# Performance work log

Measured on AMD Instinct MI355X. Metric: run time of the kernel, lower is better.

The kernel has to match this reference:

```python
import jax, jax.numpy as jnp
import numpy as np

B, S, D, F, E, NS, K = 2, 1024, 1024, 4096, 8, 8, 2
FS = F // NS  # shared-expert hidden size = d_ff // num_shared_experts


def setup_inputs() -> dict:
    key = jax.random.key(0)
    ks = jax.random.split(key, 8)
    scale = 0.02
    return {
        "hidden_states": jax.random.normal(ks[0], (B, S, D), jnp.float32),
        "gate_W": jax.random.normal(ks[1], (E, D), jnp.float32) * scale,
        "w1_e": jax.random.normal(ks[2], (E, D, F), jnp.float32) * scale,
        "w3_e": jax.random.normal(ks[3], (E, D, F), jnp.float32) * scale,
        "w2_e": jax.random.normal(ks[4], (E, F, D), jnp.float32) * scale,
        "w1_s": jax.random.normal(ks[5], (NS, D, FS), jnp.float32) * scale,
        "w3_s": jax.random.normal(ks[6], (NS, D, FS), jnp.float32) * scale,
        "w2_s": jax.random.normal(ks[7], (NS, FS, D), jnp.float32) * scale,
    }


def reference(hidden_states, gate_W, w1_e, w3_e, w2_e, w1_s, w3_s, w2_s):
    b, s, d = hidden_states.shape
    e = gate_W.shape[0]
    flat = hidden_states.reshape(-1, d)            # [T, D]
    T = flat.shape[0]

    # --- gate: softmax over experts, top-k probs scattered (k=0 slot only survives) ---
    logits = (flat @ gate_W.T).astype(jnp.float32)  # [T, E]
    probs = jax.nn.softmax(logits, axis=-1)
    top_v, top_i = jax.lax.top_k(probs, K)          # [T, K]
    gates = jnp.zeros((T, e), probs.dtype).at[jnp.arange(T)[:, None], top_i].set(top_v)

    # --- routed experts: module runs every expert densely on all tokens ---
    g = jax.nn.silu(jnp.einsum('td,edf->etf', flat, w1_e))  # [E, T, F]
    u = jnp.einsum('td,edf->etf', flat, w3_e)
    out_e = jnp.einsum('etf,efd->etd', g * u, w2_e)         # [E, T, D]
    routed = jnp.einsum('te,etd->td', gates, out_e).reshape(b, s, d)

    # --- shared experts (mean over NS experts) ---
    gs = jax.nn.silu(jnp.einsum('bsd,ndf->nbsf', hidden_states, w1_s))
    us = jnp.einsum('bsd,ndf->nbsf', hidden_states, w3_s)
    shared = jnp.einsum('nbsf,nfd->bsd', gs * us, w2_s) / w1_s.shape[0]

    alpha = 0.5
    return alpha * shared + (1.0 - alpha) * routed
```

## Files before the change

### kernel.cpp

```cpp
#include <hip/hip_runtime.h>

#define T 2048
#define D 1024
#define F 4096
#define E 8
#define NS 8
#define FS 512
#define SHB 5120
#define NROWS 7168
#define MT_MAX 56

typedef float floatx4 __attribute__((ext_vector_type(4)));
typedef short short8 __attribute__((ext_vector_type(8)));

__device__ __forceinline__ unsigned short f2bf(float f) {
  unsigned int u = __float_as_uint(f);
  u += 0x7FFF + ((u >> 16) & 1);
  return (unsigned short)(u >> 16);
}

__device__ __forceinline__ void glds16(const void* g, void* l) {
  __builtin_amdgcn_global_load_lds(
      (const __attribute__((address_space(1))) void*)g,
      (__attribute__((address_space(3))) void*)l, 16, 0, 0);
}

__global__ void gate_kernel(const float* __restrict__ x, const float* __restrict__ gW,
                            unsigned short* __restrict__ xb, int* __restrict__ cnt,
                            int* __restrict__ list_tok, float* __restrict__ list_gate) {
  int t = blockIdx.x, tid = threadIdx.x;
  const float* xr = x + (size_t)t * D;
  float acc[E];
#pragma unroll
  for (int e = 0; e < E; ++e) acc[e] = 0.f;
  for (int d = tid; d < D; d += 256) {
    float xv = xr[d];
    xb[(size_t)t * D + d] = f2bf(xv);
#pragma unroll
    for (int e = 0; e < E; ++e) acc[e] += xv * gW[e * D + d];
  }
#pragma unroll
  for (int o = 32; o > 0; o >>= 1)
#pragma unroll
    for (int e = 0; e < E; ++e) acc[e] += __shfl_down(acc[e], o, 64);
  __shared__ float wred[4][E];
  int lane = tid & 63, wv = tid >> 6;
  if (lane == 0)
#pragma unroll
    for (int e = 0; e < E; ++e) wred[wv][e] = acc[e];
  __syncthreads();
  if (tid == 0) {
    float l[E];
#pragma unroll
    for (int e = 0; e < E; ++e) l[e] = wred[0][e] + wred[1][e] + wred[2][e] + wred[3][e];
    int i1 = 0; float m1 = l[0];
    for (int e = 1; e < E; ++e) if (l[e] > m1) { m1 = l[e]; i1 = e; }
    int i2 = -1; float m2 = -3.4e38f;
    for (int e = 0; e < E; ++e) if (e != i1 && l[e] > m2) { m2 = l[e]; i2 = e; }
    float s = 0.f, p[E];
#pragma unroll
    for (int e = 0; e < E; ++e) { p[e] = __expf(l[e] - m1); s += p[e]; }
    float inv = 1.f / s;
    int p1 = atomicAdd(&cnt[i1], 1);
    list_tok[i1 * T + p1] = t; list_gate[i1 * T + p1] = p[i1] * inv;
    int p2 = atomicAdd(&cnt[i2], 1);
    list_tok[i2 * T + p2] = t; list_gate[i2 * T + p2] = p[i2] * inv;
  }
}

__global__ void offsets_kernel(const int* __restrict__ cnt, int* __restrict__ off,
                               int* __restrict__ mt_expert) {
  if (threadIdx.x == 0 && blockIdx.x == 0) {
    int o = 0;
    for (int e = 0; e < E; ++e) { off[e] = o; o += (cnt[e] + 127) & ~127; }
    off[E] = o;
    for (int i = 0; i < MT_MAX; ++i) mt_expert[i] = -1;
    for (int e = 0; e < E; ++e) {
      int t0 = off[e] >> 7, nt = (cnt[e] + 127) >> 7;
      for (int i = 0; i < nt; ++i) mt_expert[t0 + i] = e;
    }
    for (int i = SHB >> 7; i < MT_MAX; ++i) mt_expert[i] = E;
  }
}

__global__ void scatter_kernel(const int* __restrict__ cnt, const int* __restrict__ off,
                               const int* __restrict__ list_tok, const float* __restrict__ list_gate,
                               int* __restrict__ tok_of_row, float* __restrict__ row_scale,
                               int* __restrict__ tok_rows, int* __restrict__ tk) {
  int idx = blockIdx.x * 256 + threadIdx.x;
  int e = idx >> 11, i = idx & (T - 1);
  if (e < E && i < cnt[e]) {
    int row = off[e] + i;
    int t = list_tok[e * T + i];
    tok_of_row[row] = t;
    row_scale[row] = 0.5f * list_gate[e * T + i];
    int k = atomicAdd(&tk[t], 1);
    tok_rows[2 * t + k] = row;
  }
}

__global__ void transpose_cast(const float* __restrict__ in, unsigned short* __restrict__ out,
                               int R, int C) {
  in += (size_t)blockIdx.z * R * C;
  out += (size_t)blockIdx.z * R * C;
  int r0 = blockIdx.y * 32, c0 = blockIdx.x * 32;
  __shared__ float tile[32][33];
  int tid = threadIdx.x;
  {
    int rl = tid >> 3, cl = (tid & 7) * 4;
    float4 v = *(const float4*)(in + (size_t)(r0 + rl) * C + c0 + cl);
    tile[rl][cl] = v.x; tile[rl][cl + 1] = v.y;
    tile[rl][cl + 2] = v.z; tile[rl][cl + 3] = v.w;
  }
  __syncthreads();
  {
    int cl = tid >> 3, rq = (tid & 7) * 4;
    int c = c0 + cl, r = r0 + rq;
    ushort4 v;
    v.x = f2bf(tile[rq][cl]);     v.y = f2bf(tile[rq + 1][cl]);
    v.z = f2bf(tile[rq + 2][cl]); v.w = f2bf(tile[rq + 3][cl]);
    int Rt = R >> 5;
    size_t o = ((size_t)(c >> 7) * Rt + (r >> 5)) * 4096 + (size_t)(c & 127) * 32 + (r & 31);
    *(ushort4*)(out + o) = v;
  }
}

__global__ __launch_bounds__(256, 2) void up_gemm(
    const unsigned short* __restrict__ xb, const unsigned short* __restrict__ W1T,
    const unsigned short* __restrict__ W3T, const unsigned short* __restrict__ W1sT,
    const unsigned short* __restrict__ W3sT, const int* __restrict__ mt_expert,
    const int* __restrict__ tok_of_row, unsigned short* __restrict__ Hb) {
  int mt = blockIdx.y, ntile = blockIdx.x;
  int e = mt_expert[mt];
  if (e < 0) return;
  const unsigned short *B1, *B3;
  if (e < E) {
    B1 = W1T + (size_t)e * F * D;
    B3 = W3T + (size_t)e * F * D;
  } else {
    B1 = W1sT; B3 = W3sT;
  }
  __shared__ unsigned short Al0[128 * 32], B1l0[128 * 32], B3l0[128 * 32];
  __shared__ unsigned short Al1[128 * 32], B1l1[128 * 32], B3l1[128 * 32];
  int tid = threadIdx.x;
  int lane = tid & 63, wv = tid >> 6, wm = wv >> 1, wn = wv & 1;
  int row16 = lane & 15, quad = lane >> 4;
  int qsw8 = (quad ^ ((lane >> 1) & 3)) * 8;
  int swzb = (tid >> 2) * 64 + (((tid & 3) ^ ((tid >> 3) & 3)) * 16);
  int lw = wv * 1024;

  int r1 = tid >> 2;
  int hrow1 = mt * 128 + r1, hrow2 = hrow1 + 64;
  int srow1 = (e < E) ? tok_of_row[hrow1] : (hrow1 - SHB);
  int srow2 = (e < E) ? tok_of_row[hrow2] : (hrow2 - SHB);
  int asl = ((tid & 3) ^ ((tid >> 3) & 3)) * 16;
  const char* asrc1 = (const char*)(xb + (size_t)srow1 * D) + asl;
  const char* asrc2 = (const char*)(xb + (size_t)srow2 * D) + asl;
  const char* b1t = (const char*)(B1 + (size_t)ntile * (D / 32) * 4096);
  const char* b3t = (const char*)(B3 + (size_t)ntile * (D / 32) * 4096);

  floatx4 accg[4][4], accu[4][4];
#pragma unroll
  for (int i = 0; i < 4; ++i)
#pragma unroll
    for (int j = 0; j < 4; ++j) {
      accg[i][j] = (floatx4){0.f, 0.f, 0.f, 0.f};
      accu[i][j] = (floatx4){0.f, 0.f, 0.f, 0.f};
    }

  auto stage = [&](int kt, unsigned short* Ad, unsigned short* B1d, unsigned short* B3d) {
    size_t ko = (size_t)kt * 64;
    size_t bo = (size_t)kt * 8192;
    glds16(asrc1 + ko, (char*)Ad + lw);
    glds16(asrc2 + ko, (char*)Ad + 4096 + lw);
    glds16(b1t + bo + swzb, (char*)B1d + lw);
    glds16(b1t + bo + 4096 + swzb, (char*)B1d + 4096 + lw);
    glds16(b3t + bo + swzb, (char*)B3d + lw);
    glds16(b3t + bo + 4096 + swzb, (char*)B3d + 4096 + lw);
  };
  auto compute = [&](const unsigned short* Ac, const unsigned short* B1c,
                     const unsigned short* B3c) {
    short8 af[4], b1f[4], b3f[4];
#pragma unroll
    for (int mi = 0; mi < 4; ++mi)
      af[mi] = *(const short8*)(Ac + (wm * 64 + mi * 16 + row16) * 32 + qsw8);
#pragma unroll
    for (int ni = 0; ni < 4; ++ni) {
      b1f[ni] = *(const short8*)(B1c + (wn * 64 + ni * 16 + row16) * 32 + qsw8);
      b3f[ni] = *(const short8*)(B3c + (wn * 64 + ni * 16 + row16) * 32 + qsw8);
    }
#pragma unroll
    for (int mi = 0; mi < 4; ++mi)
#pragma unroll
      for (int ni = 0; ni < 4; ++ni) {
        accg[mi][ni] = __builtin_amdgcn_mfma_f32_16x16x32_bf16(af[mi], b1f[ni], accg[mi][ni], 0, 0, 0);
        accu[mi][ni] = __builtin_amdgcn_mfma_f32_16x16x32_bf16(af[mi], b3f[ni], accu[mi][ni], 0, 0, 0);
      }
  };

  stage(0, Al0, B1l0, B3l0);
  __syncthreads();
  for (int kt = 0; kt < D / 32 - 2; kt += 2) {
    stage(kt + 1, Al1, B1l1, B3l1);
    compute(Al0, B1l0, B3l0);
    __syncthreads();
    stage(kt + 2, Al0, B1l0, B3l0);
    compute(Al1, B1l1, B3l1);
    __syncthreads();
  }
  stage(D / 32 - 1, Al1, B1l1, B3l1);
  compute(Al0, B1l0, B3l0);
  __syncthreads();
  compute(Al1, B1l1, B3l1);

#pragma unroll
  for (int mi = 0; mi < 4; ++mi)
#pragma unroll
    for (int ni = 0; ni < 4; ++ni)
#pragma unroll
      for (int r = 0; r < 4; ++r) {
        int hrow = mt * 128 + wm * 64 + mi * 16 + quad * 4 + r;
        int col = ntile * 128 + wn * 64 + ni * 16 + row16;
        float g = accg[mi][ni][r], u = accu[mi][ni][r];
        float h = g * u / (1.0f + __expf(-g));
        size_t o = ((size_t)(hrow >> 7) * 128 + (col >> 5)) * 4096 + (size_t)(hrow & 127) * 32 + (col & 31);
        Hb[o] = f2bf(h);
      }
}

__global__ __launch_bounds__(256, 2) void down_gemm(
    const unsigned short* __restrict__ Hb, const unsigned short* __restrict__ W2T,
    const unsigned short* __restrict__ W2sT, const int* __restrict__ mt_expert,
    const float* __restrict__ row_scale, float* __restrict__ O) {
  int mt = blockIdx.y, ntile = blockIdx.x, kz = blockIdx.z;
  int e = mt_expert[mt];
  if (e < 0) return;
  const char* Bt = (const char*)(((e < E) ? (W2T + (size_t)e * D * F) : W2sT)
                                 + (size_t)ntile * (F / 32) * 4096);
  const char* At = (const char*)(Hb + (size_t)mt * (F / 32) * 4096);
  O += (size_t)kz * NROWS * D;
  __shared__ unsigned short Al0[128 * 32], Bl0[128 * 32];
  __shared__ unsigned short Al1[128 * 32], Bl1[128 * 32];
  int tid = threadIdx.x;
  int lane = tid & 63, wv = tid >> 6, wm = wv >> 1, wn = wv & 1;
  int row16 = lane & 15, quad = lane >> 4;
  int qsw8 = (quad ^ ((lane >> 1) & 3)) * 8;
  int swzb = (tid >> 2) * 64 + (((tid & 3) ^ ((tid >> 3) & 3)) * 16);
  int lw = wv * 1024;
  floatx4 acc[4][4];
#pragma unroll
  for (int i = 0; i < 4; ++i)
#pragma unroll
    for (int j = 0; j < 4; ++j) acc[i][j] = (floatx4){0.f, 0.f, 0.f, 0.f};

  auto stage = [&](int kt, unsigned short* Ad, unsigned short* Bd) {
    size_t o = (size_t)kt * 8192;
    glds16(At + o + swzb, (char*)Ad + lw);
    glds16(At + o + 4096 + swzb, (char*)Ad + 4096 + lw);
    glds16(Bt + o + swzb, (char*)Bd + lw);
    glds16(Bt + o + 4096 + swzb, (char*)Bd + 4096 + lw);
  };
  auto compute = [&](const unsigned short* Ac, const unsigned short* Bc) {
    short8 af[4], bf[4];
#pragma unroll
    for (int mi = 0; mi < 4; ++mi)
      af[mi] = *(const short8*)(Ac + (wm * 64 + mi * 16 + row16) * 32 + qsw8);
#pragma unroll
    for (int ni = 0; ni < 4; ++ni)
      bf[ni] = *(const short8*)(Bc + (wn * 64 + ni * 16 + row16) * 32 + qsw8);
#pragma unroll
    for (int mi = 0; mi < 4; ++mi)
#pragma unroll
      for (int ni = 0; ni < 4; ++ni)
        acc[mi][ni] = __builtin_amdgcn_mfma_f32_16x16x32_bf16(af[mi], bf[ni], acc[mi][ni], 0, 0, 0);
  };

  int k0 = kz * 64;
  stage(k0, Al0, Bl0);
  __syncthreads();
  for (int kt = k0; kt < k0 + 62; kt += 2) {
    stage(kt + 1, Al1, Bl1);
    compute(Al0, Bl0);
    __syncthreads();
    stage(kt + 2, Al0, Bl0);
    compute(Al1, Bl1);
    __syncthreads();
  }
  stage(k0 + 63, Al1, Bl1);
  compute(Al0, Bl0);
  __syncthreads();
  compute(Al1, Bl1);

#pragma unroll
  for (int mi = 0; mi < 4; ++mi)
#pragma unroll
    for (int ni = 0; ni < 4; ++ni)
#pragma unroll
      for (int r = 0; r < 4; ++r) {
        int grow = mt * 128 + wm * 64 + mi * 16 + quad * 4 + r;
        int col = ntile * 128 + wn * 64 + ni * 16 + row16;
        float scale = (grow < SHB) ? row_scale[grow] : 0.0625f;
        O[(size_t)grow * D + col] = acc[mi][ni][r] * scale;
      }
}

__global__ void combine_kernel(const float* __restrict__ O, const int* __restrict__ tok_rows,
                               float* __restrict__ out) {
  int idx = blockIdx.x * 256 + threadIdx.x;
  int t = idx >> 8, c = idx & 255;
  int r0 = tok_rows[2 * t], r1 = tok_rows[2 * t + 1];
  const float4* O4 = (const float4*)O;
  const size_t HLF = (size_t)NROWS * 256;
  float4 a = O4[(size_t)r0 * 256 + c];
  float4 b = O4[(size_t)r1 * 256 + c];
  float4 s = O4[((size_t)SHB + t) * 256 + c];
  float4 a2 = O4[HLF + (size_t)r0 * 256 + c];
  float4 b2 = O4[HLF + (size_t)r1 * 256 + c];
  float4 s2 = O4[HLF + ((size_t)SHB + t) * 256 + c];
  float4 r;
  r.x = a.x + b.x + s.x + a2.x + b2.x + s2.x;
  r.y = a.y + b.y + s.y + a2.y + b2.y + s2.y;
  r.z = a.z + b.z + s.z + a2.z + b2.z + s2.z;
  r.w = a.w + b.w + s.w + a2.w + b2.w + s2.w;
  ((float4*)out)[idx] = r;
}

extern "C" void kernel_launch(void* const* d_in, const int* in_sizes, int n_in,
                              void* d_out, int out_size, void* d_ws, size_t ws_size,
                              hipStream_t stream) {
  (void)in_sizes; (void)n_in; (void)out_size; (void)ws_size;
  const float* x   = (const float*)d_in[0];
  const float* gW  = (const float*)d_in[1];
  const float* w1e = (const float*)d_in[2];
  const float* w3e = (const float*)d_in[3];
  const float* w2e = (const float*)d_in[4];
  const float* w1s = (const float*)d_in[5];
  const float* w3s = (const float*)d_in[6];
  const float* w2s = (const float*)d_in[7];
  float* out = (float*)d_out;

  char* w = (char*)d_ws;
  auto alloc = [&](size_t bytes) {
    char* p = w; w += (bytes + 255) & ~(size_t)255; return p;
  };
  unsigned short* xb   = (unsigned short*)alloc((size_t)T * D * 2);
  unsigned short* W1T  = (unsigned short*)alloc((size_t)E * F * D * 2);
  unsigned short* W3T  = (unsigned short*)alloc((size_t)E * F * D * 2);
  unsigned short* W2T  = (unsigned short*)alloc((size_t)E * D * F * 2);
  unsigned short* W1sT = (unsigned short*)alloc((size_t)F * D * 2);
  unsigned short* W3sT = (unsigned short*)alloc((size_t)F * D * 2);
  unsigned short* W2sT = (unsigned short*)alloc((size_t)D * F * 2);
  unsigned short* Hb   = (unsigned short*)alloc((size_t)NROWS * F * 2);
  float* Ob        = (float*)alloc((size_t)2 * NROWS * D * 4);
  float* row_scale = (float*)alloc((size_t)SHB * 4);
  float* list_gate = (float*)alloc((size_t)E * T * 4);
  int* list_tok    = (int*)alloc((size_t)E * T * 4);
  int* tok_rows    = (int*)alloc((size_t)T * 2 * 4);
  int* offv        = (int*)alloc(16 * 4);
  int* mt_expert   = (int*)alloc(64 * 4);
  int* ctrl        = (int*)alloc((size_t)(8 + T + SHB) * 4);
  int* cnt = ctrl; int* tk = ctrl + 8; int* tok_of_row = ctrl + 8 + T;

  hipMemsetAsync(ctrl, 0, (size_t)(8 + T + SHB) * 4, stream);
  gate_kernel<<<T, 256, 0, stream>>>(x, gW, xb, cnt, list_tok, list_gate);
  offsets_kernel<<<1, 64, 0, stream>>>(cnt, offv, mt_expert);
  scatter_kernel<<<(E * T) / 256, 256, 0, stream>>>(cnt, offv, list_tok, list_gate,
                                                    tok_of_row, row_scale, tok_rows, tk);
  transpose_cast<<<dim3(F / 32, D / 32, E), 256, 0, stream>>>(w1e, W1T, D, F);
  transpose_cast<<<dim3(F / 32, D / 32, E), 256, 0, stream>>>(w3e, W3T, D, F);
  transpose_cast<<<dim3(D / 32, F / 32, E), 256, 0, stream>>>(w2e, W2T, F, D);
  transpose_cast<<<dim3(FS / 32, D / 32, NS), 256, 0, stream>>>(w1s, W1sT, D, FS);
  transpose_cast<<<dim3(FS / 32, D / 32, NS), 256, 0, stream>>>(w3s, W3sT, D, FS);
  transpose_cast<<<dim3(D / 32, F / 32, 1), 256, 0, stream>>>(w2s, W2sT, F, D);
  up_gemm<<<dim3(F / 128, MT_MAX), 256, 0, stream>>>(xb, W1T, W3T, W1sT, W3sT,
                                                     mt_expert, tok_of_row, Hb);
  down_gemm<<<dim3(D / 128, MT_MAX, 2), 256, 0, stream>>>(Hb, W2T, W2sT, mt_expert, row_scale, Ob);
  combine_kernel<<<(T * D / 4) / 256, 256, 0, stream>>>(Ob, tok_rows, out);
}
```

Baseline: 726.9 us.

## Triple-buffer LDS staging in up and down GEMMs with partial vmcnt waits

```diff
diff --git a/kernel.cpp b/kernel.cpp
--- a/kernel.cpp
+++ b/kernel.cpp
@@ -140,8 +140,9 @@
   } else {
     B1 = W1sT; B3 = W3sT;
   }
-  __shared__ unsigned short Al0[128 * 32], B1l0[128 * 32], B3l0[128 * 32];
-  __shared__ unsigned short Al1[128 * 32], B1l1[128 * 32], B3l1[128 * 32];
+  __shared__ unsigned short Au0[128 * 32], B1u0[128 * 32], B3u0[128 * 32];
+  __shared__ unsigned short Au1[128 * 32], B1u1[128 * 32], B3u1[128 * 32];
+  __shared__ unsigned short Au2[128 * 32], B1u2[128 * 32], B3u2[128 * 32];
   int tid = threadIdx.x;
   int lane = tid & 63, wv = tid >> 6, wm = wv >> 1, wn = wv & 1;
   int row16 = lane & 15, quad = lane >> 4;
@@ -198,20 +199,28 @@
       }
   };
 
-  stage(0, Al0, B1l0, B3l0);
-  __syncthreads();
-  for (int kt = 0; kt < D / 32 - 2; kt += 2) {
-    stage(kt + 1, Al1, B1l1, B3l1);
-    compute(Al0, B1l0, B3l0);
-    __syncthreads();
-    stage(kt + 2, Al0, B1l0, B3l0);
-    compute(Al1, B1l1, B3l1);
-    __syncthreads();
-  }
-  stage(D / 32 - 1, Al1, B1l1, B3l1);
-  compute(Al0, B1l0, B3l0);
-  __syncthreads();
-  compute(Al1, B1l1, B3l1);
+  stage(0, Au0, B1u0, B3u0);
+  stage(1, Au1, B1u1, B3u1);
+  asm volatile("s_waitcnt vmcnt(6)" ::: "memory");
+  __builtin_amdgcn_s_barrier();
+  for (int t = 0; t < 30; t += 3) {
+    stage(t + 2, Au2, B1u2, B3u2);
+    compute(Au0, B1u0, B3u0);
+    asm volatile("s_waitcnt vmcnt(6)" ::: "memory");
+    __builtin_amdgcn_s_barrier();
+    stage(t + 3, Au0, B1u0, B3u0);
+    compute(Au1, B1u1, B3u1);
+    asm volatile("s_waitcnt vmcnt(6)" ::: "memory");
+    __builtin_amdgcn_s_barrier();
+    stage(t + 4, Au1, B1u1, B3u1);
+    compute(Au2, B1u2, B3u2);
+    asm volatile("s_waitcnt vmcnt(6)" ::: "memory");
+    __builtin_amdgcn_s_barrier();
+  }
+  compute(Au0, B1u0, B3u0);
+  asm volatile("s_waitcnt vmcnt(0)" ::: "memory");
+  __builtin_amdgcn_s_barrier();
+  compute(Au1, B1u1, B3u1);
 
 #pragma unroll
   for (int mi = 0; mi < 4; ++mi)
@@ -239,8 +248,9 @@
                                  + (size_t)ntile * (F / 32) * 4096);
   const char* At = (const char*)(Hb + (size_t)mt * (F / 32) * 4096);
   O += (size_t)kz * NROWS * D;
-  __shared__ unsigned short Al0[128 * 32], Bl0[128 * 32];
-  __shared__ unsigned short Al1[128 * 32], Bl1[128 * 32];
+  __shared__ unsigned short Ad0[128 * 32], Bd0[128 * 32];
+  __shared__ unsigned short Ad1[128 * 32], Bd1[128 * 32];
+  __shared__ unsigned short Ad2[128 * 32], Bd2[128 * 32];
   int tid = threadIdx.x;
   int lane = tid & 63, wv = tid >> 6, wm = wv >> 1, wn = wv & 1;
   int row16 = lane & 15, quad = lane >> 4;
@@ -276,20 +286,36 @@
   };
 
   int k0 = kz * 64;
-  stage(k0, Al0, Bl0);
-  __syncthreads();
-  for (int kt = k0; kt < k0 + 62; kt += 2) {
-    stage(kt + 1, Al1, Bl1);
-    compute(Al0, Bl0);
-    __syncthreads();
-    stage(kt + 2, Al0, Bl0);
-    compute(Al1, Bl1);
-    __syncthreads();
-  }
-  stage(k0 + 63, Al1, Bl1);
-  compute(Al0, Bl0);
-  __syncthreads();
-  compute(Al1, Bl1);
+  stage(k0 + 0, Ad0, Bd0);
+  stage(k0 + 1, Ad1, Bd1);
+  asm volatile("s_waitcnt vmcnt(4)" ::: "memory");
+  __builtin_amdgcn_s_barrier();
+  for (int t = 0; t < 60; t += 3) {
+    stage(k0 + t + 2, Ad2, Bd2);
+    compute(Ad0, Bd0);
+    asm volatile("s_waitcnt vmcnt(4)" ::: "memory");
+    __builtin_amdgcn_s_barrier();
+    stage(k0 + t + 3, Ad0, Bd0);
+    compute(Ad1, Bd1);
+    asm volatile("s_waitcnt vmcnt(4)" ::: "memory");
+    __builtin_amdgcn_s_barrier();
+    stage(k0 + t + 4, Ad1, Bd1);
+    compute(Ad2, Bd2);
+    asm volatile("s_waitcnt vmcnt(4)" ::: "memory");
+    __builtin_amdgcn_s_barrier();
+  }
+  stage(k0 + 62, Ad2, Bd2);
+  compute(Ad0, Bd0);
+  asm volatile("s_waitcnt vmcnt(4)" ::: "memory");
+  __builtin_amdgcn_s_barrier();
+  stage(k0 + 63, Ad0, Bd0);
+  compute(Ad1, Bd1);
+  asm volatile("s_waitcnt vmcnt(4)" ::: "memory");
+  __builtin_amdgcn_s_barrier();
+  compute(Ad2, Bd2);
+  asm volatile("s_waitcnt vmcnt(0)" ::: "memory");
+  __builtin_amdgcn_s_barrier();
+  compute(Ad0, Bd0);
 
 #pragma unroll
   for (int mi = 0; mi < 4; ++mi)
```

After: 721.9 us. No clear change (-0.7%).
